# Kernel tuning notes

Hardware: AMD Instinct MI355X
Metric: run time of the kernel (lower is better)

The kernel has to match this reference:

```python
import jax, jax.numpy as jnp
import numpy as np

N = 100000
E = 3200000
IN_DIM = 768
HID = 128
NUM_CLASSES = 7


def gcn_conv(x, W, b, src, dst, n):
    """PyG GCNConv: h = D^-1/2 (A+I) D^-1/2 (x W) + b, symmetric normalization."""
    h = x @ W  # [n, out]
    loop = jnp.arange(n, dtype=src.dtype)
    s = jnp.concatenate([src, loop])  # sources (messages flow src -> dst)
    d = jnp.concatenate([dst, loop])
    deg = jax.ops.segment_sum(jnp.ones(s.shape[0], dtype=h.dtype), d, num_segments=n)
    dinv = jnp.where(deg > 0, jax.lax.rsqrt(deg), 0.0)
    norm = dinv[s] * dinv[d]  # [E+n]
    msgs = h[s] * norm[:, None]
    out = jax.ops.segment_sum(msgs, d, num_segments=n)
    return out + b


def setup_inputs() -> dict:
    key = jax.random.key(0)
    ks = jax.random.split(key, 8)
    x = jax.random.normal(ks[0], (N, IN_DIM), dtype=jnp.float32)
    edge_index = jax.random.randint(ks[1], (2, E), 0, N, dtype=jnp.int32)
    W1 = jax.random.normal(ks[2], (IN_DIM, HID), dtype=jnp.float32) / np.sqrt(IN_DIM)
    b1 = jnp.zeros((HID,), dtype=jnp.float32)
    W2 = jax.random.normal(ks[3], (HID, HID), dtype=jnp.float32) / np.sqrt(HID)
    b2 = jnp.zeros((HID,), dtype=jnp.float32)
    Wc = jax.random.normal(ks[4], (HID, NUM_CLASSES), dtype=jnp.float32) / np.sqrt(HID)
    bc = jnp.zeros((NUM_CLASSES,), dtype=jnp.float32)
    return {"x": x, "edge_index": edge_index, "W1": W1, "b1": b1,
            "W2": W2, "b2": b2, "Wc": Wc, "bc": bc}


def reference(x, edge_index, W1, b1, W2, b2, Wc, bc):
    src, dst = edge_index[0], edge_index[1]
    n = x.shape[0]
    h = jax.nn.relu(gcn_conv(x, W1, b1, src, dst, n))
    h = jax.nn.relu(gcn_conv(h, W2, b2, src, dst, n))
    logits = h @ Wc + bc
    return logits
```

## Files before the change

### kernel.cpp

```cpp
#include <hip/hip_runtime.h>
#include <hip/hip_bf16.h>

#define IN_DIM 768
#define HID 128
#define NC 7

typedef __attribute__((ext_vector_type(8))) short bf16x8;
typedef __attribute__((ext_vector_type(4))) float f32x4;

__device__ __forceinline__ ushort f2bf(float f) {
  uint u = __float_as_uint(f);
  u += 0x7fffu + ((u >> 16) & 1u);
  return (ushort)(u >> 16);
}
__device__ __forceinline__ float lof(uint v) { return __uint_as_float(v << 16); }
__device__ __forceinline__ float hif(uint v) { return __uint_as_float(v & 0xffff0000u); }
__device__ __forceinline__ uint cvtpk(float lo, float hi) {
  uint r;
  asm("v_cvt_pk_bf16_f32 %0, %1, %2" : "=v"(r) : "v"(lo), "v"(hi));
  return r;
}


__global__ __launch_bounds__(256) void k_count(const int* __restrict__ dst,
                                               int* __restrict__ cnt,
                                               int* __restrict__ pos, int E) {
  int e0 = (blockIdx.x * 256 + threadIdx.x) * 4;
  if (e0 + 4 <= E) {
    int4 d = *(const int4*)&dst[e0];
    int4 p;
    p.x = atomicAdd(&cnt[d.x], 1);
    p.y = atomicAdd(&cnt[d.y], 1);
    p.z = atomicAdd(&cnt[d.z], 1);
    p.w = atomicAdd(&cnt[d.w], 1);
    *(int4*)&pos[e0] = p;
  } else {
    for (int e = e0; e < E; ++e) pos[e] = atomicAdd(&cnt[dst[e]], 1);
  }
}

__device__ __forceinline__ int pad4(int c) { return (c + 3) & ~3; }

__global__ void k_scan_partial(const int* __restrict__ cnt, int* __restrict__ partials, int N) {
  __shared__ int sm[256];
  int b = blockIdx.x, t = threadIdx.x;
  int base = b * 1024 + t * 4;
  int s = 0;
  #pragma unroll
  for (int j = 0; j < 4; ++j) if (base + j < N) s += pad4(cnt[base + j]);
  sm[t] = s;
  __syncthreads();
  for (int off = 128; off > 0; off >>= 1) {
    if (t < off) sm[t] += sm[t + off];
    __syncthreads();
  }
  if (t == 0) partials[b] = sm[0];
}

__global__ void k_scan_combine(int* __restrict__ partials, int* __restrict__ rowptr,
                               int nch, int N) {
  __shared__ int sm[128];
  int t = threadIdx.x;
  int v0 = (t < nch) ? partials[t] : 0;
  sm[t] = v0;
  __syncthreads();
  for (int off = 1; off < 128; off <<= 1) {
    int add = (t >= off) ? sm[t - off] : 0;
    __syncthreads();
    sm[t] += add;
    __syncthreads();
  }
  if (t < nch) partials[t] = sm[t] - v0;
  if (t == 0) rowptr[N] = sm[127];
}

__global__ void k_scan_final(const int* __restrict__ cnt, const int* __restrict__ chunkoff,
                             int* __restrict__ rowptr, int N) {
  __shared__ int sm[256];
  int b = blockIdx.x, t = threadIdx.x;
  int base = b * 1024 + t * 4;
  int v[4]; int s = 0;
  #pragma unroll
  for (int j = 0; j < 4; ++j) { v[j] = (base + j < N) ? pad4(cnt[base + j]) : 0; s += v[j]; }
  sm[t] = s;
  __syncthreads();
  for (int off = 1; off < 256; off <<= 1) {
    int add = (t >= off) ? sm[t - off] : 0;
    __syncthreads();
    sm[t] += add;
    __syncthreads();
  }
  int excl = sm[t] - s;
  int run = chunkoff[b] + excl;
  #pragma unroll
  for (int j = 0; j < 4; ++j) {
    if (base + j < N) rowptr[base + j] = run;
    run += v[j];
  }
}

__global__ void k_dinv(const int* __restrict__ cnt, float* __restrict__ dinv, int N) {
  int n = blockIdx.x * 256 + threadIdx.x;
  if (n < N) dinv[n] = rsqrtf((float)(cnt[n] + 1));
}

__global__ void k_fill(int* __restrict__ p, int val, int total) {
  int i = (blockIdx.x * 256 + threadIdx.x) * 4;
  if (i + 4 <= total) {
    *(int4*)&p[i] = make_int4(val, val, val, val);
  } else {
    for (; i < total; ++i) p[i] = val;
  }
}

__global__ __launch_bounds__(256)
void k_scatter(const int* __restrict__ src, const int* __restrict__ dst,
               const int* __restrict__ pos, const int* __restrict__ rowptr,
               int* __restrict__ srcs, int E) {
  int e0 = (blockIdx.x * 256 + threadIdx.x) * 8;
  if (e0 + 8 <= E) {
    int s[8], d[8], p[8];
    *(int4*)&s[0] = *(const int4*)&src[e0];
    *(int4*)&s[4] = *(const int4*)&src[e0 + 4];
    *(int4*)&d[0] = *(const int4*)&dst[e0];
    *(int4*)&d[4] = *(const int4*)&dst[e0 + 4];
    *(int4*)&p[0] = *(const int4*)&pos[e0];
    *(int4*)&p[4] = *(const int4*)&pos[e0 + 4];
    int rp[8];
    #pragma unroll
    for (int j = 0; j < 8; ++j) rp[j] = rowptr[d[j]];
    #pragma unroll
    for (int j = 0; j < 8; ++j) srcs[rp[j] + p[j]] = s[j];
  } else {
    for (int e = e0; e < E; ++e) srcs[rowptr[dst[e]] + pos[e]] = src[e];
  }
}

__global__ void k_convW(const float* __restrict__ W, ushort* __restrict__ WT, int K) {
  int i = blockIdx.x * 256 + threadIdx.x;
  if (i >= K * HID) return;
  int k = i >> 7, c = i & 127;
  WT[c * K + k] = f2bf(W[i]);
}

__global__ __launch_bounds__(256)
void k_gemm1(const float* __restrict__ A, const ushort* __restrict__ WT,
             const float* __restrict__ dinv, ushort* __restrict__ G, const int N) {
  __shared__ ushort lB[2][128 * 64];
  const int tid = threadIdx.x;
  const int lane = tid & 63;
  const int wid = tid >> 6;
  const int lr = lane & 15, lq = lane >> 4;
  const int r0 = blockIdx.x * 64 + wid * 16;
  int arow = r0 + lr; if (arow > N - 1) arow = N - 1;
  const float* Ap = A + (size_t)arow * IN_DIM + lq * 8;

  auto stageB = [&](int buf, int k0) {
    #pragma unroll
    for (int j = 0; j < 4; ++j) {
      int i = j * 256 + tid;
      int r = i >> 3;
      int c = ((i & 7) ^ (r & 7)) * 8;
      __builtin_amdgcn_global_load_lds((const uint*)(WT + (size_t)r * IN_DIM + k0 + c),
                                       (uint*)&lB[buf][i * 8], 16, 0, 0);
    }
  };

  float4 fa[4];
  auto loadA = [&](int k0) {
    const float* p = Ap + k0;
    fa[0] = *(const float4*)p;
    fa[1] = *(const float4*)(p + 4);
    fa[2] = *(const float4*)(p + 32);
    fa[3] = *(const float4*)(p + 36);
  };

  f32x4 acc[8];
  #pragma unroll
  for (int n = 0; n < 8; ++n) acc[n] = (f32x4){0.f, 0.f, 0.f, 0.f};

  loadA(0);
  stageB(0, 0);
  __syncthreads();

  constexpr int NT = IN_DIM / 64;
  for (int t = 0; t < NT; ++t) {
    const int cur = t & 1;
    bf16x8 av[2];
    {
      uint* u = (uint*)&av[0];
      u[0] = cvtpk(fa[0].x, fa[0].y); u[1] = cvtpk(fa[0].z, fa[0].w);
      u[2] = cvtpk(fa[1].x, fa[1].y); u[3] = cvtpk(fa[1].z, fa[1].w);
      u[4] = cvtpk(fa[2].x, fa[2].y); u[5] = cvtpk(fa[2].z, fa[2].w);
      u[6] = cvtpk(fa[3].x, fa[3].y); u[7] = cvtpk(fa[3].z, fa[3].w);
    }
    if (t + 1 < NT) { loadA((t + 1) * 64); stageB(cur ^ 1, (t + 1) * 64); }
    #pragma unroll
    for (int kk = 0; kk < 2; ++kk) {
      #pragma unroll
      for (int n = 0; n < 8; ++n) {
        int C = n * 16 + lr;
        int slot = (kk * 4 + lq) ^ (C & 7);
        bf16x8 bv = *(const bf16x8*)&lB[cur][C * 64 + slot * 8];
        acc[n] = __builtin_amdgcn_mfma_f32_16x16x32_bf16(av[kk], bv, acc[n], 0, 0, 0);
      }
    }
    __syncthreads();
  }

  float dv[4];
  #pragma unroll
  for (int i = 0; i < 4; ++i) {
    int row = r0 + lq * 4 + i;
    dv[i] = (row < N) ? dinv[row] : 0.f;
  }
  #pragma unroll
  for (int n = 0; n < 8; ++n) {
    #pragma unroll
    for (int i = 0; i < 4; ++i) {
      int row = r0 + lq * 4 + i;
      if (row < N) G[(size_t)row * HID + n * 16 + lr] = f2bf(dv[i] * acc[n][i]);
    }
  }
}

__global__ __launch_bounds__(256)
void k_gemm2(const ushort* __restrict__ A, const ushort* __restrict__ WT,
             const float* __restrict__ dinv, ushort* __restrict__ G, const int N) {
  __shared__ ushort lA[2][128 * 64];
  __shared__ ushort lB[2][128 * 64];
  const int tid = threadIdx.x;
  const int lane = tid & 63;
  const int wid = tid >> 6;
  const int wm = wid >> 1, wn = wid & 1;
  const int row0 = blockIdx.x * 128;
  const int lr = lane & 15;
  const int lk8 = lane >> 4;
  constexpr int K = HID;

  auto stage = [&](int buf, int k0) {
    #pragma unroll
    for (int j = 0; j < 4; ++j) {
      int i = j * 256 + tid;
      int r = i >> 3;
      int c = ((i & 7) ^ (r & 7)) * 8;
      int ga = row0 + r; ga = ga < N ? ga : N - 1;
      __builtin_amdgcn_global_load_lds((const uint*)(A + (size_t)ga * K + k0 + c),
                                       (uint*)&lA[buf][i * 8], 16, 0, 0);
      __builtin_amdgcn_global_load_lds((const uint*)(WT + (size_t)r * K + k0 + c),
                                       (uint*)&lB[buf][i * 8], 16, 0, 0);
    }
  };

  f32x4 acc[4][4];
  #pragma unroll
  for (int m = 0; m < 4; ++m)
    #pragma unroll
    for (int n = 0; n < 4; ++n)
      acc[m][n] = (f32x4){0.f, 0.f, 0.f, 0.f};

  constexpr int NT = K / 64;
  stage(0, 0);
  __syncthreads();

  for (int t = 0; t < NT; ++t) {
    const int cur = t & 1;
    if (t + 1 < NT) stage(cur ^ 1, (t + 1) * 64);
    #pragma unroll
    for (int kk = 0; kk < 2; ++kk) {
      bf16x8 av[4], bv[4];
      #pragma unroll
      for (int m = 0; m < 4; ++m) {
        int R = wm * 64 + m * 16 + lr;
        int slot = (kk * 4 + lk8) ^ (R & 7);
        av[m] = *(const bf16x8*)&lA[cur][R * 64 + slot * 8];
      }
      #pragma unroll
      for (int n = 0; n < 4; ++n) {
        int C = wn * 64 + n * 16 + lr;
        int slot = (kk * 4 + lk8) ^ (C & 7);
        bv[n] = *(const bf16x8*)&lB[cur][C * 64 + slot * 8];
      }
      #pragma unroll
      for (int m = 0; m < 4; ++m)
        #pragma unroll
        for (int n = 0; n < 4; ++n)
          acc[m][n] = __builtin_amdgcn_mfma_f32_16x16x32_bf16(av[m], bv[n], acc[m][n], 0, 0, 0);
    }
    __syncthreads();
  }

  #pragma unroll
  for (int m = 0; m < 4; ++m) {
    #pragma unroll
    for (int i = 0; i < 4; ++i) {
      int row = row0 + wm * 64 + m * 16 + (lane >> 4) * 4 + i;
      if (row < N) {
        float dv = dinv[row];
        #pragma unroll
        for (int n = 0; n < 4; ++n) {
          int col = wn * 64 + n * 16 + lr;
          G[(size_t)row * HID + col] = f2bf(dv * acc[m][n][i]);
        }
      }
    }
  }
}


#define GL(v, s) uint v = Gp[(size_t)(s) * 64 + lane];
#define AC(v) { a0 += lof(v); a1 += hif(v); }

__device__ __forceinline__ void agg32(const uint* __restrict__ Gp,
                                      const int* __restrict__ srcs,
                                      int i, int lane, float& a0, float& a1) {
  int4 sa = *(const int4*)&srcs[i];
  int4 sb = *(const int4*)&srcs[i + 4];
  int4 sc = *(const int4*)&srcs[i + 8];
  int4 sd = *(const int4*)&srcs[i + 12];
  int4 se = *(const int4*)&srcs[i + 16];
  int4 sf = *(const int4*)&srcs[i + 20];
  int4 sg = *(const int4*)&srcs[i + 24];
  int4 sh = *(const int4*)&srcs[i + 28];
  GL(h00, sa.x) GL(h01, sa.y) GL(h02, sa.z) GL(h03, sa.w)
  GL(h04, sb.x) GL(h05, sb.y) GL(h06, sb.z) GL(h07, sb.w)
  GL(h08, sc.x) GL(h09, sc.y) GL(h10, sc.z) GL(h11, sc.w)
  GL(h12, sd.x) GL(h13, sd.y) GL(h14, sd.z) GL(h15, sd.w)
  GL(h16, se.x) GL(h17, se.y) GL(h18, se.z) GL(h19, se.w)
  GL(h20, sf.x) GL(h21, sf.y) GL(h22, sf.z) GL(h23, sf.w)
  GL(h24, sg.x) GL(h25, sg.y) GL(h26, sg.z) GL(h27, sg.w)
  GL(h28, sh.x) GL(h29, sh.y) GL(h30, sh.z) GL(h31, sh.w)
  __builtin_amdgcn_sched_barrier(0);
  AC(h00) AC(h01) AC(h02) AC(h03) AC(h04) AC(h05) AC(h06) AC(h07)
  AC(h08) AC(h09) AC(h10) AC(h11) AC(h12) AC(h13) AC(h14) AC(h15)
  AC(h16) AC(h17) AC(h18) AC(h19) AC(h20) AC(h21) AC(h22) AC(h23)
  AC(h24) AC(h25) AC(h26) AC(h27) AC(h28) AC(h29) AC(h30) AC(h31)
}

__device__ __forceinline__ void agg16(const uint* __restrict__ Gp,
                                      const int* __restrict__ srcs,
                                      int i, int lane, float& a0, float& a1) {
  int4 sa = *(const int4*)&srcs[i];
  int4 sb = *(const int4*)&srcs[i + 4];
  int4 sc = *(const int4*)&srcs[i + 8];
  int4 sd = *(const int4*)&srcs[i + 12];
  GL(h00, sa.x) GL(h01, sa.y) GL(h02, sa.z) GL(h03, sa.w)
  GL(h04, sb.x) GL(h05, sb.y) GL(h06, sb.z) GL(h07, sb.w)
  GL(h08, sc.x) GL(h09, sc.y) GL(h10, sc.z) GL(h11, sc.w)
  GL(h12, sd.x) GL(h13, sd.y) GL(h14, sd.z) GL(h15, sd.w)
  __builtin_amdgcn_sched_barrier(0);
  AC(h00) AC(h01) AC(h02) AC(h03) AC(h04) AC(h05) AC(h06) AC(h07)
  AC(h08) AC(h09) AC(h10) AC(h11) AC(h12) AC(h13) AC(h14) AC(h15)
}

__device__ __forceinline__ void agg4(const uint* __restrict__ Gp,
                                     const int* __restrict__ srcs,
                                     int i, int lane, float& a0, float& a1) {
  int4 sa = *(const int4*)&srcs[i];
  GL(h00, sa.x) GL(h01, sa.y) GL(h02, sa.z) GL(h03, sa.w)
  __builtin_amdgcn_sched_barrier(0);
  AC(h00) AC(h01) AC(h02) AC(h03)
}

__global__ __launch_bounds__(256)
void k_agg(const uint* __restrict__ Gp, const int* __restrict__ srcs,
           const int* __restrict__ rowptr, const float* __restrict__ dinv,
           const float* __restrict__ bias, uint* __restrict__ Ou, int N) {
  int w = (blockIdx.x * 256 + threadIdx.x) >> 6;
  if (w >= N) return;
  int lane = threadIdx.x & 63;
  int start = rowptr[w], end = rowptr[w + 1];
  float di = dinv[w];
  uint hv = Gp[(size_t)w * 64 + lane];
  float a0 = lof(hv), a1 = hif(hv);
  int i = start;
  for (; i + 32 <= end; i += 32) agg32(Gp, srcs, i, lane, a0, a1);
  for (; i + 16 <= end; i += 16) agg16(Gp, srcs, i, lane, a0, a1);
  for (; i < end; i += 4)        agg4(Gp, srcs, i, lane, a0, a1);
  float2 bb = ((const float2*)bias)[lane];
  a0 = fmaxf(fmaf(di, a0, bb.x), 0.f);
  a1 = fmaxf(fmaf(di, a1, bb.y), 0.f);
  Ou[(size_t)w * 64 + lane] = (uint)f2bf(a0) | ((uint)f2bf(a1) << 16);
}

__global__ __launch_bounds__(256)
void k_agg_final(const uint* __restrict__ Gp, const int* __restrict__ srcs,
                 const int* __restrict__ rowptr, const float* __restrict__ dinv,
                 const float* __restrict__ bias, const float* __restrict__ Wc,
                 const float* __restrict__ bc, float* __restrict__ out, int N) {
  int w = (blockIdx.x * 256 + threadIdx.x) >> 6;
  if (w >= N) return;
  int lane = threadIdx.x & 63;
  int start = rowptr[w], end = rowptr[w + 1];
  float di = dinv[w];
  uint hv = Gp[(size_t)w * 64 + lane];
  float a0 = lof(hv), a1 = hif(hv);
  int i = start;
  for (; i + 32 <= end; i += 32) agg32(Gp, srcs, i, lane, a0, a1);
  for (; i + 16 <= end; i += 16) agg16(Gp, srcs, i, lane, a0, a1);
  for (; i < end; i += 4)        agg4(Gp, srcs, i, lane, a0, a1);
  float2 bb = ((const float2*)bias)[lane];
  a0 = fmaxf(fmaf(di, a0, bb.x), 0.f);
  a1 = fmaxf(fmaf(di, a1, bb.y), 0.f);
  const float* w0 = &Wc[(2 * lane) * NC];
  #pragma unroll
  for (int c = 0; c < NC; ++c) {
    float s = a0 * w0[c] + a1 * w0[NC + c];
    #pragma unroll
    for (int off = 32; off > 0; off >>= 1) s += __shfl_xor(s, off, 64);
    if (lane == 0) out[(size_t)w * NC + c] = s + bc[c];
  }
}

extern "C" void kernel_launch(void* const* d_in, const int* in_sizes, int n_in,
                              void* d_out, int out_size, void* d_ws, size_t ws_size,
                              hipStream_t stream) {
  const float* x  = (const float*)d_in[0];
  const int*   ei = (const int*)d_in[1];
  const float* W1 = (const float*)d_in[2];
  const float* b1 = (const float*)d_in[3];
  const float* W2 = (const float*)d_in[4];
  const float* b2 = (const float*)d_in[5];
  const float* Wc = (const float*)d_in[6];
  const float* bc = (const float*)d_in[7];
  float* out = (float*)d_out;

  const int N = in_sizes[0] / IN_DIM;
  const int E = in_sizes[1] / 2;
  const int* src = ei;
  const int* dst = ei + E;
  const int CSRCAP = E + 3 * N + 64;

  char* ws = (char*)d_ws;
  size_t off = 0;
  auto alloc = [&](size_t bytes) -> void* {
    off = (off + 255) & ~(size_t)255;
    void* p = ws + off;
    off += bytes;
    return p;
  };
  ushort* H0     = (ushort*)alloc((size_t)(N + 1) * HID * 2);
  ushort* H1     = (ushort*)alloc((size_t)(N + 1) * HID * 2);
  int*    srcs   = (int*)alloc((size_t)CSRCAP * 4);
  int*    cnt    = (int*)alloc((size_t)N * 4);
  int*    pos    = (int*)alloc((size_t)E * 4);
  int*    rowptr = (int*)alloc((size_t)(N + 1) * 4);
  float*  dinv   = (float*)alloc((size_t)N * 4);
  int*    partials = (int*)alloc(512);
  ushort* W1T    = (ushort*)alloc((size_t)IN_DIM * HID * 2);
  ushort* W2T    = (ushort*)alloc((size_t)HID * HID * 2);

  hipMemsetAsync(cnt, 0, (size_t)N * 4, stream);
  hipMemsetAsync(H0 + (size_t)N * HID, 0, HID * 2, stream);

  k_convW<<<(IN_DIM * HID + 255) / 256, 256, 0, stream>>>(W1, W1T, IN_DIM);
  k_convW<<<(HID * HID + 255) / 256, 256, 0, stream>>>(W2, W2T, HID);

  k_count<<<(E + 1023) / 1024, 256, 0, stream>>>(dst, cnt, pos, E);
  int nch = (N + 1023) >> 10;
  k_scan_partial<<<nch, 256, 0, stream>>>(cnt, partials, N);
  k_scan_combine<<<1, 128, 0, stream>>>(partials, rowptr, nch, N);
  k_scan_final<<<nch, 256, 0, stream>>>(cnt, partials, rowptr, N);
  k_dinv<<<(N + 255) / 256, 256, 0, stream>>>(cnt, dinv, N);
  k_fill<<<(CSRCAP + 1023) / 1024, 256, 0, stream>>>(srcs, N, CSRCAP);
  k_scatter<<<(E + 2047) / 2048, 256, 0, stream>>>(src, dst, pos, rowptr, srcs, E);

  k_gemm1<<<(N + 63) / 64, 256, 0, stream>>>(x, W1T, dinv, H0, N);
  k_agg<<<(N + 3) / 4, 256, 0, stream>>>((const uint*)H0, srcs, rowptr, dinv, b1,
                                         (uint*)H1, N);
  k_gemm2<<<(N + 127) / 128, 256, 0, stream>>>(H1, W2T, dinv, H0, N);
  k_agg_final<<<(N + 3) / 4, 256, 0, stream>>>((const uint*)H0, srcs, rowptr, dinv, b2,
                                               Wc, bc, out, N);
}
```

Baseline: 581.3 us.

## Bucket CSR neighbor lists by source-index group for gather locality

Counts edges per (destination, source-group) pair, where each group covers 8192 consecutive source ids. A per-row scan turns these counts into offsets, so each destination's neighbor list comes out partially sorted by source group. The goal is better cache locality in the feature gathers during aggregation. In exchange it adds a larger counter array of N*NG ints to memset, an extra rowscan kernel, and one more indirect load per edge in the scatter.

```diff
diff --git a/kernel.cpp b/kernel.cpp
--- a/kernel.cpp
+++ b/kernel.cpp
@@ -4,6 +4,7 @@
 #define IN_DIM 768
 #define HID 128
 #define NC 7
+#define GSH 13
 
 typedef __attribute__((ext_vector_type(8))) short bf16x8;
 typedef __attribute__((ext_vector_type(4))) float f32x4;
@@ -22,21 +23,37 @@
 }
 
 
-__global__ __launch_bounds__(256) void k_count(const int* __restrict__ dst,
-                                               int* __restrict__ cnt,
-                                               int* __restrict__ pos, int E) {
+__global__ __launch_bounds__(256) void k_count(const int* __restrict__ src,
+                                               const int* __restrict__ dst,
+                                               int* __restrict__ cnt2,
+                                               int* __restrict__ pos, int E, int NG) {
   int e0 = (blockIdx.x * 256 + threadIdx.x) * 4;
   if (e0 + 4 <= E) {
-    int4 d = *(const int4*)&dst[e0];
+    int4 s4 = *(const int4*)&src[e0];
+    int4 d4 = *(const int4*)&dst[e0];
     int4 p;
-    p.x = atomicAdd(&cnt[d.x], 1);
-    p.y = atomicAdd(&cnt[d.y], 1);
-    p.z = atomicAdd(&cnt[d.z], 1);
-    p.w = atomicAdd(&cnt[d.w], 1);
+    p.x = atomicAdd(&cnt2[d4.x * NG + (s4.x >> GSH)], 1);
+    p.y = atomicAdd(&cnt2[d4.y * NG + (s4.y >> GSH)], 1);
+    p.z = atomicAdd(&cnt2[d4.z * NG + (s4.z >> GSH)], 1);
+    p.w = atomicAdd(&cnt2[d4.w * NG + (s4.w >> GSH)], 1);
     *(int4*)&pos[e0] = p;
   } else {
-    for (int e = e0; e < E; ++e) pos[e] = atomicAdd(&cnt[dst[e]], 1);
-  }
+    for (int e = e0; e < E; ++e)
+      pos[e] = atomicAdd(&cnt2[dst[e] * NG + (src[e] >> GSH)], 1);
+  }
+}
+
+__global__ __launch_bounds__(256) void k_rowscan(int* __restrict__ cnt2,
+                                                 int* __restrict__ cnt, int N, int NG) {
+  int n = blockIdx.x * 256 + threadIdx.x;
+  if (n >= N) return;
+  int s = 0;
+  for (int g = 0; g < NG; ++g) {
+    int b = cnt2[n * NG + g];
+    cnt2[n * NG + g] = s;
+    s += b;
+  }
+  cnt[n] = s;
 }
 
 __device__ __forceinline__ int pad4(int c) { return (c + 3) & ~3; }
@@ -116,7 +133,7 @@
 __global__ __launch_bounds__(256)
 void k_scatter(const int* __restrict__ src, const int* __restrict__ dst,
                const int* __restrict__ pos, const int* __restrict__ rowptr,
-               int* __restrict__ srcs, int E) {
+               const int* __restrict__ base2, int* __restrict__ srcs, int E, int NG) {
   int e0 = (blockIdx.x * 256 + threadIdx.x) * 8;
   if (e0 + 8 <= E) {
     int s[8], d[8], p[8];
@@ -126,13 +143,18 @@
     *(int4*)&d[4] = *(const int4*)&dst[e0 + 4];
     *(int4*)&p[0] = *(const int4*)&pos[e0];
     *(int4*)&p[4] = *(const int4*)&pos[e0 + 4];
-    int rp[8];
+    int rp[8], gb[8];
     #pragma unroll
     for (int j = 0; j < 8; ++j) rp[j] = rowptr[d[j]];
     #pragma unroll
-    for (int j = 0; j < 8; ++j) srcs[rp[j] + p[j]] = s[j];
+    for (int j = 0; j < 8; ++j) gb[j] = base2[d[j] * NG + (s[j] >> GSH)];
+    #pragma unroll
+    for (int j = 0; j < 8; ++j) srcs[rp[j] + gb[j] + p[j]] = s[j];
   } else {
-    for (int e = e0; e < E; ++e) srcs[rowptr[dst[e]] + pos[e]] = src[e];
+    for (int e = e0; e < E; ++e) {
+      int ss = src[e], dd = dst[e];
+      srcs[rowptr[dd] + base2[dd * NG + (ss >> GSH)] + pos[e]] = ss;
+    }
   }
 }
 
@@ -429,6 +451,7 @@
   const int E = in_sizes[1] / 2;
   const int* src = ei;
   const int* dst = ei + E;
+  const int NG = ((N - 1) >> GSH) + 1;
   const int CSRCAP = E + 3 * N + 64;
 
   char* ws = (char*)d_ws;
@@ -442,6 +465,7 @@
   ushort* H0     = (ushort*)alloc((size_t)(N + 1) * HID * 2);
   ushort* H1     = (ushort*)alloc((size_t)(N + 1) * HID * 2);
   int*    srcs   = (int*)alloc((size_t)CSRCAP * 4);
+  int*    cnt2   = (int*)alloc((size_t)N * NG * 4);
   int*    cnt    = (int*)alloc((size_t)N * 4);
   int*    pos    = (int*)alloc((size_t)E * 4);
   int*    rowptr = (int*)alloc((size_t)(N + 1) * 4);
@@ -450,20 +474,21 @@
   ushort* W1T    = (ushort*)alloc((size_t)IN_DIM * HID * 2);
   ushort* W2T    = (ushort*)alloc((size_t)HID * HID * 2);
 
-  hipMemsetAsync(cnt, 0, (size_t)N * 4, stream);
+  hipMemsetAsync(cnt2, 0, (size_t)N * NG * 4, stream);
   hipMemsetAsync(H0 + (size_t)N * HID, 0, HID * 2, stream);
 
   k_convW<<<(IN_DIM * HID + 255) / 256, 256, 0, stream>>>(W1, W1T, IN_DIM);
   k_convW<<<(HID * HID + 255) / 256, 256, 0, stream>>>(W2, W2T, HID);
 
-  k_count<<<(E + 1023) / 1024, 256, 0, stream>>>(dst, cnt, pos, E);
+  k_count<<<(E + 1023) / 1024, 256, 0, stream>>>(src, dst, cnt2, pos, E, NG);
+  k_rowscan<<<(N + 255) / 256, 256, 0, stream>>>(cnt2, cnt, N, NG);
   int nch = (N + 1023) >> 10;
   k_scan_partial<<<nch, 256, 0, stream>>>(cnt, partials, N);
   k_scan_combine<<<1, 128, 0, stream>>>(partials, rowptr, nch, N);
   k_scan_final<<<nch, 256, 0, stream>>>(cnt, partials, rowptr, N);
   k_dinv<<<(N + 255) / 256, 256, 0, stream>>>(cnt, dinv, N);
   k_fill<<<(CSRCAP + 1023) / 1024, 256, 0, stream>>>(srcs, N, CSRCAP);
-  k_scatter<<<(E + 2047) / 2048, 256, 0, stream>>>(src, dst, pos, rowptr, srcs, E);
+  k_scatter<<<(E + 2047) / 2048, 256, 0, stream>>>(src, dst, pos, rowptr, cnt2, srcs, E, NG);
 
   k_gemm1<<<(N + 63) / 64, 256, 0, stream>>>(x, W1T, dinv, H0, N);
   k_agg<<<(N + 3) / 4, 256, 0, stream>>>((const uint*)H0, srcs, rowptr, dinv, b1,
```

After: 608.6 us. 1.05x slower.
